# Performance work log

Measured on AMD Instinct MI355X. Metric: run time of the kernel, lower is better.

Reference implementation:

```python
import jax, jax.numpy as jnp
import numpy as np

D = 1024      # d_model
H = 16        # n_heads
HD = D // H   # head_dim = 64
B = 2
T = 2048


def setup_inputs() -> dict:
    key = jax.random.key(0)
    k0, k1, k2 = jax.random.split(key, 3)
    s = 1.0 / np.sqrt(D)
    return {
        "x": jax.random.normal(k0, (B, T, D), dtype=jnp.float32),
        "qkv_w": jax.random.normal(k1, (D, 3 * D), dtype=jnp.float32) * s,
        "qkv_b": jnp.zeros((3 * D,), dtype=jnp.float32),
        "out_w": jax.random.normal(k2, (D, D), dtype=jnp.float32) * s,
        "out_b": jnp.zeros((D,), dtype=jnp.float32),
    }


def _apply_rotary(x, rope):
    # Faithful to the torch apply_rotary: even/odd interleaved split of both
    # x and the [sin(freqs)|cos(freqs)] rope table.
    x1, x2 = x[..., ::2], x[..., 1::2]
    sin, cos = rope[..., ::2], rope[..., 1::2]
    return jnp.concatenate([x1 * cos - x2 * sin, x1 * sin + x2 * cos], axis=-1)


def reference(x, qkv_w, qkv_b, out_w, out_b):
    Bx, Tx, Dm = x.shape
    # QKV projection -> [3, B, H, T, HD]
    qkv = (x @ qkv_w + qkv_b).reshape(Bx, Tx, 3, H, HD).transpose(2, 0, 3, 1, 4)
    q, k, v = qkv[0], qkv[1], qkv[2]

    # Rotary table: rope = concat(sin(freqs), cos(freqs)) along last dim -> [T, HD]
    inv_freq = 1.0 / (10000.0 ** (jnp.arange(0, HD, 2, dtype=jnp.float32) / HD))
    t = jnp.arange(Tx, dtype=jnp.float32)
    freqs = t[:, None] * inv_freq[None, :]          # [T, HD/2]
    rope = jnp.concatenate([jnp.sin(freqs), jnp.cos(freqs)], axis=-1)  # [T, HD]

    q = _apply_rotary(q, rope)
    k = _apply_rotary(k, rope)

    scale = HD ** -0.5
    scores = jnp.einsum('bhqd,bhkd->bhqk', q, k) * scale  # [B,H,T,T]
    causal_mask = jnp.triu(jnp.ones((Tx, Tx), dtype=bool), 1)
    scores = jnp.where(causal_mask, -jnp.inf, scores)
    attn = jax.nn.softmax(scores, axis=-1)
    # dropout is identity in eval mode
    out = jnp.einsum('bhqk,bhkd->bhqd', attn, v)           # [B,H,T,HD]
    out = out.transpose(0, 2, 1, 3).reshape(Bx, Tx, Dm)    # [B,T,D]
    return out @ out_w + out_b
```

## Files before the change

kernel.cpp:

```cpp
#include <hip/hip_runtime.h>

typedef unsigned short u16;
typedef __attribute__((ext_vector_type(8))) __bf16 bf16x8;
typedef __attribute__((ext_vector_type(4))) float f32x4;

#define NB 2
#define NT 2048
#define ND 1024
#define NH 16
#define HD 64

__device__ __forceinline__ float b2f(u16 u) {
  union { float f; unsigned int i; } v; v.i = ((unsigned int)u) << 16; return v.f;
}
__device__ __forceinline__ u16 f2b(float f) {
  union { float f; unsigned int i; } v; v.f = f;
  unsigned int r = (v.i + 0x7FFFu + ((v.i >> 16) & 1u)) >> 16;
  return (u16)r;
}

__device__ __forceinline__ void gload_lds16(const u16* g, u16* lds) {
  __builtin_amdgcn_global_load_lds(
      (const __attribute__((address_space(1))) unsigned int*)(g),
      (__attribute__((address_space(3))) unsigned int*)(lds),
      16, 0, 0);
}

__device__ __forceinline__ f32x4 mfma16(bf16x8 a, bf16x8 b, f32x4 c) {
  return __builtin_amdgcn_mfma_f32_16x16x32_bf16(a, b, c, 0, 0, 0);
}

template <int N>
__device__ __forceinline__ float ror16(float x) {
  return __int_as_float(__builtin_amdgcn_update_dpp(
      __float_as_int(x), __float_as_int(x), 0x120 | N, 0xF, 0xF, true));
}
__device__ __forceinline__ float rsum16(float x) {
  x += ror16<8>(x);
  x += ror16<4>(x);
  x += ror16<2>(x);
  x += ror16<1>(x);
  return x;
}

__device__ __forceinline__ float fast_sin(float a) {
  float r = a * 0.15915494309189535f;
  r -= floorf(r);
  return __builtin_amdgcn_sinf(r);
}
__device__ __forceinline__ float fast_cos(float a) {
  float r = a * 0.15915494309189535f;
  r -= floorf(r);
  return __builtin_amdgcn_cosf(r);
}

__global__ __launch_bounds__(256) void cast_f32_bf16(const float* __restrict__ in,
                                                     u16* __restrict__ out, int n) {
  int i = (blockIdx.x * 256 + threadIdx.x) * 8;
  if (i + 8 <= n) {
#pragma unroll
    for (int j = 0; j < 8; ++j) out[i + j] = f2b(in[i + j]);
  }
}

__global__ __launch_bounds__(256) void transpose_cast(const float* __restrict__ in,
                                                      u16* __restrict__ out,
                                                      int K, int N) {
  __shared__ u16 tile[32][33];
  int n0 = blockIdx.x * 32, k0 = blockIdx.y * 32;
  int tx = threadIdx.x, ty = threadIdx.y;
  for (int i = ty; i < 32; i += 8)
    tile[i][tx] = f2b(in[(size_t)(k0 + i) * N + n0 + tx]);
  __syncthreads();
  for (int i = ty; i < 32; i += 8)
    out[(size_t)(n0 + i) * K + k0 + tx] = tile[tx][i];
}

template <int BM, bool F32OUT>
__global__ __launch_bounds__(256) void gemm_bt(const u16* __restrict__ A,
                                               const u16* __restrict__ Bt,
                                               const float* __restrict__ bias,
                                               void* __restrict__ Cv,
                                               int M, int N, int K) {
  constexpr int MI = BM / 32;
  __shared__ alignas(16) u16 As[BM * 32];
  __shared__ alignas(16) u16 Bs[128 * 32];
  const int tid = threadIdx.x;
  const int lane = tid & 63;
  const int wave = tid >> 6;
  const int l15 = lane & 15, quad = lane >> 4;
  const int wm = (wave >> 1) * (BM / 2), wn = (wave & 1) * 64;
  const int row0 = blockIdx.y * BM, col0 = blockIdx.x * 128;

  f32x4 acc[MI][4] = {};

  for (int k0 = 0; k0 < K; k0 += 32) {
    __syncthreads();
#pragma unroll
    for (int p = 0; p < BM / 64; ++p) {
      int idx8 = p * 256 + tid;
      int r = idx8 >> 2, c = (idx8 & 3) * 8;
      gload_lds16(&A[(size_t)(row0 + r) * K + k0 + c], &As[idx8 * 8]);
    }
#pragma unroll
    for (int p = 0; p < 2; ++p) {
      int idx8 = p * 256 + tid;
      int r = idx8 >> 2, c = (idx8 & 3) * 8;
      gload_lds16(&Bt[(size_t)(col0 + r) * K + k0 + c], &Bs[idx8 * 8]);
    }
    __syncthreads();
    bf16x8 af[MI], bfr[4];
#pragma unroll
    for (int mi = 0; mi < MI; ++mi)
      af[mi] = *(const bf16x8*)&As[(wm + mi * 16 + l15) * 32 + quad * 8];
#pragma unroll
    for (int ni = 0; ni < 4; ++ni)
      bfr[ni] = *(const bf16x8*)&Bs[(wn + ni * 16 + l15) * 32 + quad * 8];
#pragma unroll
    for (int mi = 0; mi < MI; ++mi)
#pragma unroll
      for (int ni = 0; ni < 4; ++ni)
        acc[mi][ni] = mfma16(af[mi], bfr[ni], acc[mi][ni]);
  }

#pragma unroll
  for (int ni = 0; ni < 4; ++ni) {
    int c = col0 + wn + ni * 16 + l15;
    float bv = bias[c];
#pragma unroll
    for (int mi = 0; mi < MI; ++mi) {
      int r0 = row0 + wm + mi * 16 + quad * 4;
      f32x4 v = acc[mi][ni];
#pragma unroll
      for (int r = 0; r < 4; ++r) {
        if (F32OUT)
          ((float*)Cv)[(size_t)(r0 + r) * N + c] = v[r] + bv;
        else
          ((u16*)Cv)[(size_t)(r0 + r) * N + c] = f2b(v[r] + bv);
      }
    }
  }
}

__global__ __launch_bounds__(256) void prep_frag(const u16* __restrict__ qkv,
                                                 u16* __restrict__ qsw,
                                                 u16* __restrict__ ksw,
                                                 u16* __restrict__ vsw) {
  __shared__ u16 tq[32 * 72];
  __shared__ u16 tk[32 * 72];
  __shared__ u16 tv[32 * 72];
  const int bh = blockIdx.y;
  const int b = bh >> 4, h = bh & 15;
  const int t0 = blockIdx.x * 32;
  const int tid = threadIdx.x;

  {
    int row = tid >> 3, col = (tid & 7) * 8;
    const u16* src = &qkv[(size_t)(b * NT + t0 + row) * 3072 + h * HD + col];
    *(bf16x8*)&tq[row * 72 + col] = *(const bf16x8*)src;
    *(bf16x8*)&tk[row * 72 + col] = *(const bf16x8*)(src + ND);
    *(bf16x8*)&tv[row * 72 + col] = *(const bf16x8*)(src + 2 * ND);
  }
  __syncthreads();

  {
    const int isK = tid >> 7;
    const int chunk = (tid >> 4) & 7;
    const int tl = tid & 15;
    const int ks = chunk >> 2, quad = chunk & 3;
    const u16* tile = isK ? tk : tq;
    u16* dst = isK ? ksw : qsw;
    const float scale = isK ? 1.0f : 0.125f;
    const float LOG1E4 = 9.210340371976184f;

#pragma unroll
    for (int rbloc = 0; rbloc < 2; ++rbloc) {
      const int row = rbloc * 16 + tl;
      const float tf = (float)(t0 + row);
      union { u16 s[8]; bf16x8 v; } o;
#pragma unroll
      for (int e = 0; e < 8; ++e) {
        int c = ks * 32 + quad * 8 + e;
        int j = c & 31;
        int c1 = 2 * j, c2 = 2 * j + 1;
        float inv1 = __expf(-((float)(c1 & 31)) * (1.0f / 32.0f) * LOG1E4);
        float inv2 = __expf(-((float)(c2 & 31)) * (1.0f / 32.0f) * LOG1E4);
        float a1 = tf * inv1, a2 = tf * inv2;
        float sA = (c1 < 32) ? fast_sin(a1) : fast_cos(a1);
        float cA = (c2 < 32) ? fast_sin(a2) : fast_cos(a2);
        float x1 = b2f(tile[row * 72 + c1]), x2 = b2f(tile[row * 72 + c2]);
        float ov = (c < 32) ? (x1 * cA - x2 * sA) : (x1 * sA + x2 * cA);
        o.s[e] = f2b(ov * scale);
      }
      size_t addr =
          ((((size_t)bh * 128 + (t0 >> 4) + rbloc) * 2 + ks) * 64 + quad * 16 + tl) * 8;
      *(bf16x8*)&dst[addr] = o.v;
    }
  }

  {
    const int ni = tid >> 6, lane = tid & 63;
    const int quad = lane >> 4, l15 = lane & 15;
    union { u16 s[8]; bf16x8 v; } o;
#pragma unroll
    for (int e = 0; e < 8; ++e)
      o.s[e] = tv[(quad * 8 + e) * 72 + ni * 16 + l15];
    *(bf16x8*)&vsw[(((size_t)bh * 64 + (t0 >> 5)) * 4 + ni) * 512 + lane * 8] = o.v;
  }
}

__global__ __launch_bounds__(128, 2) void flash_kernel(const u16* __restrict__ qsw,
                                                       const u16* __restrict__ ksw,
                                                       const u16* __restrict__ vsw,
                                                       u16* __restrict__ attn) {
  __shared__ alignas(16) u16 Ps[2 * 5120];
  __shared__ float Ll[32];

  const int tid = threadIdx.x;
  const int w = tid >> 6;
  const int lane = tid & 63;
  const int l15 = lane & 15, quad = lane >> 4;
  const int linear = (int)blockIdx.x;
  const int bh = linear & 31;
  const int qt = 63 - (linear >> 5);
  const int r0 = qt * 32;
  u16* Psw = &Ps[w * 5120];

  bf16x8 aq[2][2];
#pragma unroll
  for (int mi = 0; mi < 2; ++mi)
#pragma unroll
    for (int ks = 0; ks < 2; ++ks)
      aq[mi][ks] = *(const bf16x8*)&qsw[
          ((((size_t)bh * 128 + qt * 2 + mi) * 2 + ks) * 64 + lane) * 8];

  f32x4 oacc[2][4] = {};
  float lst[8] = {0.f, 0.f, 0.f, 0.f, 0.f, 0.f, 0.f, 0.f};

  const int ktmax = qt >> 2;
  for (int kt = w; kt <= ktmax; kt += 2) {
    bf16x8 kf[2][8];
#pragma unroll
    for (int ks = 0; ks < 2; ++ks)
#pragma unroll
      for (int ni = 0; ni < 8; ++ni)
        kf[ks][ni] = *(const bf16x8*)&ksw[
            ((((size_t)bh * 128 + kt * 8 + ni) * 2 + ks) * 64 + lane) * 8];

    f32x4 sacc[2][8] = {};
#pragma unroll
    for (int ks = 0; ks < 2; ++ks)
#pragma unroll
      for (int ni = 0; ni < 8; ++ni) {
        sacc[0][ni] = mfma16(aq[0][ks], kf[ks][ni], sacc[0][ni]);
        sacc[1][ni] = mfma16(aq[1][ks], kf[ks][ni], sacc[1][ni]);
      }

    bf16x8 vf[4][4];
#pragma unroll
    for (int ks = 0; ks < 4; ++ks)
#pragma unroll
      for (int ni = 0; ni < 4; ++ni)
        vf[ks][ni] = *(const bf16x8*)&vsw[
            (((size_t)bh * 64 + kt * 4 + ks) * 4 + ni) * 512 + lane * 8];

    const bool diag = (kt == ktmax);
    const int k0 = kt * 128;
#pragma unroll
    for (int mi = 0; mi < 2; ++mi)
#pragma unroll
      for (int r = 0; r < 4; ++r) {
        const int prow = mi * 16 + quad * 4 + r;
        float sv[8];
#pragma unroll
        for (int ni = 0; ni < 8; ++ni) sv[ni] = sacc[mi][ni][r];
        if (diag) {
#pragma unroll
          for (int ni = 0; ni < 8; ++ni)
            if (k0 + ni * 16 + l15 > r0 + prow) sv[ni] = -__builtin_inff();
        }
        float rs = 0.f;
#pragma unroll
        for (int ni = 0; ni < 8; ++ni) {
          float p = __expf(sv[ni]);
          sv[ni] = p;
          rs += p;
        }
        lst[mi * 4 + r] += rsum16(rs);
#pragma unroll
        for (int ni = 0; ni < 8; ++ni)
          Psw[(ni >> 1) * 1280 + prow * 40 + (ni & 1) * 16 + l15] = f2b(sv[ni]);
      }

    asm volatile("" ::: "memory");

#pragma unroll
    for (int ks = 0; ks < 4; ++ks) {
      bf16x8 ap0 = *(const bf16x8*)&Psw[ks * 1280 + l15 * 40 + quad * 8];
      bf16x8 ap1 = *(const bf16x8*)&Psw[ks * 1280 + (16 + l15) * 40 + quad * 8];
#pragma unroll
      for (int ni = 0; ni < 4; ++ni) {
        oacc[0][ni] = mfma16(ap0, vf[ks][ni], oacc[0][ni]);
        oacc[1][ni] = mfma16(ap1, vf[ks][ni], oacc[1][ni]);
      }
    }
  }

  float* Of = (float*)&Ps[5120];
  if (w == 1) {
#pragma unroll
    for (int mi = 0; mi < 2; ++mi)
#pragma unroll
      for (int r = 0; r < 4; ++r) {
        const int row = mi * 16 + quad * 4 + r;
        if (l15 == 0) Ll[row] = lst[mi * 4 + r];
#pragma unroll
        for (int ni = 0; ni < 4; ++ni)
          Of[row * 64 + ni * 16 + l15] = oacc[mi][ni][r];
      }
  }
  __syncthreads();
  if (w == 0) {
    const int b = bh >> 4, h = bh & 15;
#pragma unroll
    for (int mi = 0; mi < 2; ++mi)
#pragma unroll
      for (int r = 0; r < 4; ++r) {
        const int row = mi * 16 + quad * 4 + r;
        const float rl = 1.0f / (lst[mi * 4 + r] + Ll[row]);
        const int trow = r0 + row;
#pragma unroll
        for (int ni = 0; ni < 4; ++ni) {
          float o = oacc[mi][ni][r] + Of[row * 64 + ni * 16 + l15];
          attn[((size_t)b * NT + trow) * ND + h * HD + ni * 16 + l15] = f2b(o * rl);
        }
      }
  }
}

extern "C" void kernel_launch(void* const* d_in, const int* in_sizes, int n_in,
                              void* d_out, int out_size, void* d_ws, size_t ws_size,
                              hipStream_t stream) {
  const float* x = (const float*)d_in[0];
  const float* qkv_w = (const float*)d_in[1];
  const float* qkv_b = (const float*)d_in[2];
  const float* out_w = (const float*)d_in[3];
  const float* out_b = (const float*)d_in[4];
  float* out = (float*)d_out;

  u16* ws = (u16*)d_ws;
  u16* xb    = ws;
  u16* wqkvT = xb + (size_t)4096 * 1024;
  u16* woutT = wqkvT + 3072 * 1024;
  u16* qkv   = woutT + 1024 * 1024;
  u16* qsw   = qkv + (size_t)4096 * 3072;
  u16* ksw   = qsw + (size_t)32 * 2048 * 64;
  u16* vsw   = ksw + (size_t)32 * 2048 * 64;
  u16* attn  = vsw + (size_t)32 * 2048 * 64;

  cast_f32_bf16<<<(NB * NT * ND) / (256 * 8), 256, 0, stream>>>(
      x, xb, NB * NT * ND);

  transpose_cast<<<dim3(3 * ND / 32, ND / 32), dim3(32, 8), 0, stream>>>(
      qkv_w, wqkvT, ND, 3 * ND);
  transpose_cast<<<dim3(ND / 32, ND / 32), dim3(32, 8), 0, stream>>>(
      out_w, woutT, ND, ND);

  gemm_bt<128, false><<<dim3(3 * ND / 128, NB * NT / 128), 256, 0, stream>>>(
      xb, wqkvT, qkv_b, qkv, NB * NT, 3 * ND, ND);

  prep_frag<<<dim3(NT / 32, NB * NH), 256, 0, stream>>>(qkv, qsw, ksw, vsw);

  flash_kernel<<<dim3(2048), 128, 0, stream>>>(qsw, ksw, vsw, attn);

  gemm_bt<64, true><<<dim3(ND / 128, NB * NT / 64), 256, 0, stream>>>(
      attn, woutT, out_b, out, NB * NT, ND, ND);
}
```

Baseline: 192.3 us.

## Replace QKV projection GEMM with 256x256 tiled, 8-wave pipelined kernel

Adds a new bf16 GEMM kernel with 256x256 block tiles, 512 threads, XOR-swizzled LDS staged via direct global-to-LDS loads, and a four-phase schedule. Each phase is bracketed by barriers and s_setprio so the loads for the next tiles overlap the MFMA work. The QKV projection launch switches to this kernel to get more reuse per tile and hide memory latency. The cost is a large 128KB LDS footprint and a grid of only 192 blocks, which may underfill the CUs. The hand-placed waitcnt and barrier ordering also makes correctness fragile.

```diff
diff --git a/kernel.cpp b/kernel.cpp
--- a/kernel.cpp
+++ b/kernel.cpp
@@ -142,6 +142,140 @@
   }
 }
 
+__device__ __forceinline__ void stage_half(const u16* __restrict__ g, int ldk,
+                                           u16* l, int tid) {
+#pragma unroll
+  for (int p = 0; p < 2; ++p) {
+    int idx = p * 512 + tid;
+    int r = idx >> 3;
+    int c = (idx & 7) ^ (r & 7);
+    gload_lds16(&g[(size_t)r * ldk + c * 8], &l[idx * 8]);
+  }
+}
+
+#define AH(b, h) (&lds[((b) * 2 + (h)) * 8192])
+#define BH(b, h) (&lds[32768 + ((b) * 2 + (h)) * 8192])
+
+#define LOAD_AF(base)                                                       \
+  _Pragma("unroll") for (int mm = 0; mm < 4; ++mm) {                        \
+    af[mm][0] = *(const bf16x8*)&(base)[arow + mm * 2048 + swz0];           \
+    af[mm][1] = *(const bf16x8*)&(base)[arow + mm * 2048 + swz1];           \
+  }
+#define LOAD_BF(base)                                                       \
+  _Pragma("unroll") for (int nn = 0; nn < 2; ++nn) {                        \
+    bfr[nn][0] = *(const bf16x8*)&(base)[brow + nn * 4096 + swz0];          \
+    bfr[nn][1] = *(const bf16x8*)&(base)[brow + nn * 4096 + swz1];          \
+  }
+#define MFMA_Q(MA, NQ)                                                      \
+  _Pragma("unroll") for (int mm = 0; mm < 4; ++mm)                          \
+  _Pragma("unroll") for (int nn = 0; nn < 2; ++nn) {                        \
+    acc[(MA) * 4 + mm][(NQ) * 2 + nn] =                                     \
+        mfma16(af[mm][0], bfr[nn][0], acc[(MA) * 4 + mm][(NQ) * 2 + nn]);   \
+    acc[(MA) * 4 + mm][(NQ) * 2 + nn] =                                     \
+        mfma16(af[mm][1], bfr[nn][1], acc[(MA) * 4 + mm][(NQ) * 2 + nn]);   \
+  }
+#define PH_SYNC                                                             \
+  __builtin_amdgcn_s_barrier();                                             \
+  asm volatile("s_waitcnt lgkmcnt(0)");                                     \
+  __builtin_amdgcn_sched_barrier(0);                                        \
+  __builtin_amdgcn_s_setprio(1);
+#define PH_END                                                              \
+  __builtin_amdgcn_s_setprio(0);                                            \
+  __builtin_amdgcn_s_barrier();                                             \
+  asm volatile("" ::: "memory");
+
+__global__ __launch_bounds__(512, 2) void gemm256_bt(const u16* __restrict__ A,
+                                                     const u16* __restrict__ Bt,
+                                                     const float* __restrict__ bias,
+                                                     u16* __restrict__ C,
+                                                     int M, int N, int K) {
+  __shared__ alignas(16) u16 lds[65536];
+  const int tid = threadIdx.x;
+  const int lane = tid & 63;
+  const int wave = tid >> 6;
+  const int l15 = lane & 15, quad = lane >> 4;
+  const int wm = wave >> 2, wn = wave & 3;
+  const int row0 = blockIdx.y * 256, col0 = blockIdx.x * 256;
+  const int NTIL = K >> 6;
+
+  const u16* Ag0 = A + (size_t)row0 * K;
+  const u16* Ag1 = Ag0 + (size_t)128 * K;
+  const u16* Bg0 = Bt + (size_t)col0 * K;
+  const u16* Bg1 = Bg0 + (size_t)128 * K;
+
+  const int swz0 = (quad ^ (l15 & 7)) * 8;
+  const int swz1 = ((4 + quad) ^ (l15 & 7)) * 8;
+  const int arow = (wm * 16 + l15) * 64;
+  const int brow = (wn * 16 + l15) * 64;
+
+  f32x4 acc[8][4] = {};
+
+  stage_half(Bg0, K, BH(0, 0), tid);
+  stage_half(Ag1, K, AH(0, 1), tid);
+  stage_half(Ag0, K, AH(0, 0), tid);
+  stage_half(Bg1, K, BH(0, 1), tid);
+  {
+    int tp = (NTIL > 1) ? 1 : 0;
+    stage_half(Bg0 + tp * 64, K, BH(1, 0), tid);
+    stage_half(Ag1 + tp * 64, K, AH(1, 1), tid);
+  }
+  asm volatile("s_waitcnt vmcnt(4)");
+  __builtin_amdgcn_s_barrier();
+  asm volatile("" ::: "memory");
+
+  bf16x8 af[4][2], bfr[2][2];
+#pragma unroll 2
+  for (int t = 0; t < NTIL; ++t) {
+    const int cur = t & 1, nxt = cur ^ 1;
+    const int t1 = (t + 1 < NTIL) ? t + 1 : NTIL - 1;
+    const int t2 = (t + 2 < NTIL) ? t + 2 : NTIL - 1;
+    u16* Ac0 = AH(cur, 0);
+    u16* Ac1 = AH(cur, 1);
+    u16* Bc0 = BH(cur, 0);
+    u16* Bc1 = BH(cur, 1);
+
+    LOAD_AF(Ac0);
+    LOAD_BF(Bc0);
+    stage_half(Ag0 + t1 * 64, K, AH(nxt, 0), tid);
+    PH_SYNC; MFMA_Q(0, 0); PH_END;
+
+    LOAD_AF(Ac1);
+    stage_half(Bg1 + t1 * 64, K, BH(nxt, 1), tid);
+    PH_SYNC; MFMA_Q(1, 0); PH_END;
+
+    LOAD_BF(Bc1);
+    stage_half(Bg0 + t2 * 64, K, Bc0, tid);
+    PH_SYNC; MFMA_Q(1, 1); PH_END;
+
+    LOAD_AF(Ac0);
+    stage_half(Ag1 + t2 * 64, K, Ac1, tid);
+    __builtin_amdgcn_s_barrier();
+    asm volatile("s_waitcnt lgkmcnt(0)");
+    __builtin_amdgcn_sched_barrier(0);
+    __builtin_amdgcn_s_setprio(1);
+    MFMA_Q(0, 1);
+    __builtin_amdgcn_s_setprio(0);
+    asm volatile("s_waitcnt vmcnt(4)");
+    __builtin_amdgcn_s_barrier();
+    asm volatile("" ::: "memory");
+  }
+  asm volatile("s_waitcnt vmcnt(0)");
+
+#pragma unroll
+  for (int ni = 0; ni < 4; ++ni) {
+    const int col = col0 + (ni >> 1) * 128 + (ni & 1) * 64 + wn * 16 + l15;
+    const float bv = bias[col];
+#pragma unroll
+    for (int mi = 0; mi < 8; ++mi) {
+      const int r0 = row0 + (mi >> 2) * 128 + (mi & 3) * 32 + wm * 16 + quad * 4;
+      f32x4 v = acc[mi][ni];
+#pragma unroll
+      for (int rr = 0; rr < 4; ++rr)
+        C[(size_t)(r0 + rr) * N + col] = f2b(v[rr] + bv);
+    }
+  }
+}
+
 __global__ __launch_bounds__(256) void prep_frag(const u16* __restrict__ qkv,
                                                  u16* __restrict__ qsw,
                                                  u16* __restrict__ ksw,
@@ -366,7 +500,7 @@
   transpose_cast<<<dim3(ND / 32, ND / 32), dim3(32, 8), 0, stream>>>(
       out_w, woutT, ND, ND);
 
-  gemm_bt<128, false><<<dim3(3 * ND / 128, NB * NT / 128), 256, 0, stream>>>(
+  gemm256_bt<<<dim3(3 * ND / 256, NB * NT / 256), 512, 0, stream>>>(
       xb, wqkvT, qkv_b, qkv, NB * NT, 3 * ND, ND);
 
   prep_frag<<<dim3(NT / 32, NB * NH), 256, 0, stream>>>(qkv, qsw, ksw, vsw);
```

After: 190.2 us. No clear change (-1.1%).
